# Performance work log

Hardware: AMD Instinct MI355X
Metric: run time of the kernel (lower is better)

The kernel has to match this reference:

```python
import jax, jax.numpy as jnp
import numpy as np

D_MODEL = 512
D_INNER = 1024   # expand * d_model
D_STATE = 16
D_CONV = 4
DT_RANK = 32     # ceil(d_model / 16)
N_LAYERS = 4
N_PRED_LAYERS = 2
FEAT = 128
LN_EPS = 1e-5


def _ln(x, w, b):
    m = x.mean(-1, keepdims=True)
    v = ((x - m) ** 2).mean(-1, keepdims=True)
    return (x - m) * jax.lax.rsqrt(v + LN_EPS) * w + b


def _silu(x):
    return x * jax.nn.sigmoid(x)


def _causal_conv(x, w, b):
    # depthwise causal conv1d: x (B,L,C), w (C,K), b (C,)
    K = w.shape[1]
    L = x.shape[1]
    xp = jnp.pad(x, ((0, 0), (K - 1, 0), (0, 0)))
    y = b
    for k in range(K):
        y = y + xp[:, k:k + L, :] * w[:, k]
    return y


def _mamba(x, in_w, conv_w, conv_b, xp_w, dt_w, dt_b, Alog, Dp, out_w):
    # x: (B,L,d_model)
    xz = jnp.einsum('bld,ed->ble', x, in_w)          # (B,L,2*d_inner)
    xi, z = jnp.split(xz, 2, axis=-1)
    xc = _silu(_causal_conv(xi, conv_w, conv_b))     # (B,L,d_inner)
    dbc = jnp.einsum('blc,ec->ble', xc, xp_w)        # (B,L,dt_rank+2N)
    dt = dbc[..., :DT_RANK]
    Bm = dbc[..., DT_RANK:DT_RANK + D_STATE]         # (B,L,N)
    Cm = dbc[..., DT_RANK + D_STATE:]                # (B,L,N)
    delta = jax.nn.softplus(jnp.einsum('blr,cr->blc', dt, dt_w) + dt_b)  # (B,L,d_inner)
    A = -jnp.exp(Alog)                               # (d_inner,N), negative
    dA = jnp.exp(delta[..., None] * A)               # (B,L,d_inner,N)
    dBu = delta[..., None] * Bm[:, :, None, :] * xc[..., None]

    def step(h, inp):
        dA_t, dBu_t, C_t = inp
        h = dA_t * h + dBu_t                         # (B,d_inner,N)
        y = jnp.einsum('bcn,bn->bc', h, C_t)
        return h, y

    h0 = jnp.zeros((x.shape[0], D_INNER, D_STATE), x.dtype)
    _, ys = jax.lax.scan(step, h0, (dA.transpose(1, 0, 2, 3),
                                    dBu.transpose(1, 0, 2, 3),
                                    Cm.transpose(1, 0, 2)))
    y = ys.transpose(1, 0, 2) + Dp * xc              # skip connection D*u
    y = y * _silu(z)
    return jnp.einsum('blc,dc->bld', y, out_w)


def _forward(x, inp_w, inp_b, enc_ln_w, enc_ln_b, enc_in_w, enc_conv_w, enc_conv_b,
             enc_xp_w, enc_dt_w, enc_dt_b, enc_Alog, enc_D, enc_out_w,
             fin_ln_w, fin_ln_b, prd_ln_w, prd_ln_b, prd_in_w, prd_conv_w, prd_conv_b,
             prd_xp_w, prd_dt_w, prd_dt_b, prd_Alog, prd_D, prd_out_w,
             prd_nrm_w, prd_nrm_b, prd_proj_w, prd_proj_b):
    # MambaEncoder: input_proj + n_layers pre-norm residual Mamba blocks + final LN
    h = jnp.einsum('blf,df->bld', x, inp_w) + inp_b
    for i in range(N_LAYERS):
        h = h + _mamba(_ln(h, enc_ln_w[i], enc_ln_b[i]),
                       enc_in_w[i], enc_conv_w[i], enc_conv_b[i], enc_xp_w[i],
                       enc_dt_w[i], enc_dt_b[i], enc_Alog[i], enc_D[i], enc_out_w[i])
    ctx = _ln(h, fin_ln_w, fin_ln_b)
    # MambaPredictor: small causal mamba stack + norm + proj
    p = ctx
    for i in range(N_PRED_LAYERS):
        p = p + _mamba(_ln(p, prd_ln_w[i], prd_ln_b[i]),
                       prd_in_w[i], prd_conv_w[i], prd_conv_b[i], prd_xp_w[i],
                       prd_dt_w[i], prd_dt_b[i], prd_Alog[i], prd_D[i], prd_out_w[i])
    p = _ln(p, prd_nrm_w, prd_nrm_b)
    preds = jnp.einsum('bld,ed->ble', p, prd_proj_w) + prd_proj_b
    return preds


def _mamba_params(key, n, scale=0.02):
    ks = jax.random.split(key, 6)
    arange_A = jnp.tile(jnp.log(jnp.arange(1, D_STATE + 1, dtype=jnp.float32)), (n, D_INNER, 1))
    return dict(
        in_w=jax.random.normal(ks[0], (n, 2 * D_INNER, D_MODEL)) * scale,
        conv_w=jax.random.normal(ks[1], (n, D_INNER, D_CONV)) * scale,
        conv_b=jnp.zeros((n, D_INNER)),
        xp_w=jax.random.normal(ks[2], (n, DT_RANK + 2 * D_STATE, D_INNER)) * scale,
        dt_w=jax.random.normal(ks[3], (n, D_INNER, DT_RANK)) * scale,
        dt_b=jnp.full((n, D_INNER), jnp.log(jnp.expm1(0.01))),  # inv-softplus(0.01)
        Alog=arange_A,
        D=jnp.ones((n, D_INNER)),
        out_w=jax.random.normal(ks[4], (n, D_MODEL, D_INNER)) * scale,
    )


def setup_inputs() -> dict:
    key = jax.random.key(0)
    ks = jax.random.split(key, 8)
    enc = _mamba_params(ks[0], N_LAYERS)
    prd = _mamba_params(ks[1], N_PRED_LAYERS)
    return {
        'x': jax.random.normal(ks[2], (2, 1024, FEAT), dtype=jnp.float32),
        'inp_w': jax.random.normal(ks[3], (D_MODEL, FEAT)) * 0.02,
        'inp_b': jnp.zeros((D_MODEL,)),
        'enc_ln_w': jnp.ones((N_LAYERS, D_MODEL)), 'enc_ln_b': jnp.zeros((N_LAYERS, D_MODEL)),
        'enc_in_w': enc['in_w'], 'enc_conv_w': enc['conv_w'], 'enc_conv_b': enc['conv_b'],
        'enc_xp_w': enc['xp_w'], 'enc_dt_w': enc['dt_w'], 'enc_dt_b': enc['dt_b'],
        'enc_Alog': enc['Alog'], 'enc_D': enc['D'], 'enc_out_w': enc['out_w'],
        'fin_ln_w': jnp.ones((D_MODEL,)), 'fin_ln_b': jnp.zeros((D_MODEL,)),
        'prd_ln_w': jnp.ones((N_PRED_LAYERS, D_MODEL)), 'prd_ln_b': jnp.zeros((N_PRED_LAYERS, D_MODEL)),
        'prd_in_w': prd['in_w'], 'prd_conv_w': prd['conv_w'], 'prd_conv_b': prd['conv_b'],
        'prd_xp_w': prd['xp_w'], 'prd_dt_w': prd['dt_w'], 'prd_dt_b': prd['dt_b'],
        'prd_Alog': prd['Alog'], 'prd_D': prd['D'], 'prd_out_w': prd['out_w'],
        'prd_nrm_w': jnp.ones((D_MODEL,)), 'prd_nrm_b': jnp.zeros((D_MODEL,)),
        'prd_proj_w': jax.random.normal(ks[4], (D_MODEL, D_MODEL)) * 0.02,
        'prd_proj_b': jnp.zeros((D_MODEL,)),
    }


def reference(x, inp_w, inp_b, enc_ln_w, enc_ln_b, enc_in_w, enc_conv_w, enc_conv_b,
              enc_xp_w, enc_dt_w, enc_dt_b, enc_Alog, enc_D, enc_out_w,
              fin_ln_w, fin_ln_b, prd_ln_w, prd_ln_b, prd_in_w, prd_conv_w, prd_conv_b,
              prd_xp_w, prd_dt_w, prd_dt_b, prd_Alog, prd_D, prd_out_w,
              prd_nrm_w, prd_nrm_b, prd_proj_w, prd_proj_b):
    return _forward(x, inp_w, inp_b, enc_ln_w, enc_ln_b, enc_in_w, enc_conv_w, enc_conv_b,
                    enc_xp_w, enc_dt_w, enc_dt_b, enc_Alog, enc_D, enc_out_w,
                    fin_ln_w, fin_ln_b, prd_ln_w, prd_ln_b, prd_in_w, prd_conv_w, prd_conv_b,
                    prd_xp_w, prd_dt_w, prd_dt_b, prd_Alog, prd_D, prd_out_w,
                    prd_nrm_w, prd_nrm_b, prd_proj_w, prd_proj_b)
```

## Files before the change

### kernel.cpp

```cpp
#include <hip/hip_runtime.h>
#include <hip/hip_bf16.h>

using bf16 = __hip_bfloat16;
typedef __attribute__((ext_vector_type(8))) short short8;
typedef __attribute__((ext_vector_type(4))) float f32x4;
typedef __attribute__((ext_vector_type(4))) unsigned int uint4v;

static constexpr int LB = 2;
static constexpr int LL = 1024;
static constexpr int DM = 512;
static constexpr int DI = 1024;
static constexpr int DSN = 16;
static constexpr int RK = 32;
static constexpr int MR_ROWS = LB * LL;

struct ConvArgs {
    const float* src[9];
    bf16*        dst[9];
    int          n4[9];
};

__global__ __launch_bounds__(256) void convert_bf16_multi(ConvArgs a) {
    const int s = blockIdx.y;
    const float4* __restrict__ src = (const float4*)a.src[s];
    bf16* __restrict__ dst = a.dst[s];
    const int n4 = a.n4[s];
    for (int i = blockIdx.x * 256 + threadIdx.x; i < n4; i += gridDim.x * 256) {
        float4 v = src[i];
        bf16 t[4] = {__float2bfloat16(v.x), __float2bfloat16(v.y),
                     __float2bfloat16(v.z), __float2bfloat16(v.w)};
        *(uint2*)(dst + (size_t)i * 4) = *(uint2*)t;
    }
}

__device__ __forceinline__ void ln_store(float* outrow, int tid, float a, float b) {
    ((float2*)outrow)[tid] = make_float2(a, b);
}
__device__ __forceinline__ void ln_store(bf16* outrow, int tid, float a, float b) {
    __hip_bfloat162 h;
    h.x = __float2bfloat16(a);
    h.y = __float2bfloat16(b);
    ((__hip_bfloat162*)outrow)[tid] = h;
}

template <typename T>
__global__ __launch_bounds__(256) void ln_kernel(const float* __restrict__ x,
                                                 const float* __restrict__ w,
                                                 const float* __restrict__ b,
                                                 T* __restrict__ out) {
    const int row = blockIdx.x;
    const int tid = threadIdx.x;
    const int wid = tid >> 6, lane = tid & 63;
    __shared__ float red[8];

    const float2 v = ((const float2*)(x + (size_t)row * DM))[tid];
    float s = v.x + v.y;
#pragma unroll
    for (int m = 1; m < 64; m <<= 1) s += __shfl_xor(s, m);
    if (lane == 0) red[wid] = s;
    __syncthreads();
    const float mean = (red[0] + red[1] + red[2] + red[3]) * (1.f / DM);
    const float d0 = v.x - mean, d1 = v.y - mean;
    float s2 = d0 * d0 + d1 * d1;
#pragma unroll
    for (int m = 1; m < 64; m <<= 1) s2 += __shfl_xor(s2, m);
    if (lane == 0) red[4 + wid] = s2;
    __syncthreads();
    const float var = (red[4] + red[5] + red[6] + red[7]) * (1.f / DM);
    const float rs = rsqrtf(var + 1e-5f);
    const float2 wv = ((const float2*)w)[tid];
    const float2 bv = ((const float2*)b)[tid];
    ln_store(out + (size_t)row * DM, tid, d0 * rs * wv.x + bv.x, d1 * rs * wv.y + bv.y);
}

template <int BM, int BN, int BK, int EPI>
__global__ __launch_bounds__(256) void gemm_bt(const bf16* __restrict__ A, int lda,
                                               const bf16* __restrict__ B, int ldb,
                                               float* __restrict__ C, int ldc,
                                               int K, const float* __restrict__ bias) {
    static_assert(BK == 64, "swizzle assumes 128B LDS row stride");
    constexpr int MR = (BM / 2) / 16;
    constexpr int NR = (BN / 2) / 16;
    __shared__ __align__(16) bf16 sA[BM * BK];
    __shared__ __align__(16) bf16 sB[BN * BK];

    const int tid = threadIdx.x;
    const int lane = tid & 63, wid = tid >> 6;
    const int wr = wid >> 1, wc = wid & 1;
    const int m0 = blockIdx.y * BM, n0 = blockIdx.x * BN;

    f32x4 acc[MR][NR] = {};

    constexpr int A_LD = BM * BK * 2 / (256 * 16);
    constexpr int B_LD = BN * BK * 2 / (256 * 16);
    static_assert(A_LD >= 1 && B_LD >= 1, "tile too small");

    for (int k0 = 0; k0 < K; k0 += BK) {
#pragma unroll
        for (int i = 0; i < A_LD; ++i) {
            const int byte = (tid + i * 256) * 16;
            const int row = byte / (BK * 2), colb = byte % (BK * 2);
            const int sw = colb ^ ((row & 7) << 4);
            *(uint4v*)((char*)sA + row * (BK * 2) + sw) =
                *(const uint4v*)((const char*)A + ((size_t)(m0 + row) * lda + k0) * 2 + colb);
        }
#pragma unroll
        for (int i = 0; i < B_LD; ++i) {
            const int byte = (tid + i * 256) * 16;
            const int row = byte / (BK * 2), colb = byte % (BK * 2);
            const int sw = colb ^ ((row & 7) << 4);
            *(uint4v*)((char*)sB + row * (BK * 2) + sw) =
                *(const uint4v*)((const char*)B + ((size_t)(n0 + row) * ldb + k0) * 2 + colb);
        }
        __syncthreads();
#pragma unroll
        for (int kk = 0; kk < BK; kk += 32) {
            const int kb2 = (kk + (lane >> 4) * 8) * 2;
            short8 af[MR], bfr[NR];
#pragma unroll
            for (int m = 0; m < MR; ++m) {
                const int r = wr * (BM / 2) + m * 16 + (lane & 15);
                af[m] = *(const short8*)((const char*)sA + r * (BK * 2) + (kb2 ^ ((r & 7) << 4)));
            }
#pragma unroll
            for (int n = 0; n < NR; ++n) {
                const int r = wc * (BN / 2) + n * 16 + (lane & 15);
                bfr[n] = *(const short8*)((const char*)sB + r * (BK * 2) + (kb2 ^ ((r & 7) << 4)));
            }
#pragma unroll
            for (int m = 0; m < MR; ++m) {
#pragma unroll
                for (int n = 0; n < NR; ++n) {
                    acc[m][n] = __builtin_amdgcn_mfma_f32_16x16x32_bf16(af[m], bfr[n], acc[m][n], 0, 0, 0);
                }
            }
        }
        __syncthreads();
    }

#pragma unroll
    for (int m = 0; m < MR; ++m) {
#pragma unroll
        for (int n = 0; n < NR; ++n) {
            const int col = n0 + wc * (BN / 2) + n * 16 + (lane & 15);
            const float bv = (EPI == 1) ? bias[col] : 0.f;
#pragma unroll
            for (int j = 0; j < 4; ++j) {
                const int row = m0 + wr * (BM / 2) + m * 16 + (lane >> 4) * 4 + j;
                float v = acc[m][n][j] + bv;
                float* p = C + (size_t)row * ldc + col;
                if (EPI == 3) v += *p;
                *p = v;
            }
        }
    }
}

__global__ __launch_bounds__(256) void conv_silu_T(const float* __restrict__ xz,
                                                   const float* __restrict__ cw,
                                                   const float* __restrict__ cb,
                                                   bf16* __restrict__ xc_bf,
                                                   float* __restrict__ xc_t,
                                                   float* __restrict__ zs_t) {
    const int c0 = blockIdx.x * 64;
    const int r0 = blockIdx.y * 64;
    const int bstart = (r0 >> 10) << 10;
    const int tid = threadIdx.x;

    __shared__ float sx[67 * 64];
    __shared__ float T[64 * 65];

    for (int idx = tid; idx < 67 * 16; idx += 256) {
        const int rr = idx >> 4, f4 = idx & 15;
        const int row = r0 - 3 + rr;
        float4 v = make_float4(0.f, 0.f, 0.f, 0.f);
        if (row >= bstart)
            v = *(const float4*)(xz + (size_t)row * (2 * DI) + c0 + f4 * 4);
        *(float4*)(sx + rr * 64 + f4 * 4) = v;
    }
    __syncthreads();

    const int c = tid & 63;
    const int rgrp = tid >> 6;
    const float4 w = *(const float4*)(cw + (size_t)(c0 + c) * 4);
    const float cbv = cb[c0 + c];
#pragma unroll
    for (int i = 0; i < 16; ++i) {
        const int r = rgrp + i * 4;
        float acc = cbv + w.w * sx[(r + 3) * 64 + c] + w.z * sx[(r + 2) * 64 + c]
                        + w.y * sx[(r + 1) * 64 + c] + w.x * sx[(r + 0) * 64 + c];
        const float s = acc / (1.f + expf(-acc));
        xc_bf[(size_t)(r0 + r) * DI + c0 + c] = __float2bfloat16(s);
        T[c * 65 + r] = s;
    }
    __syncthreads();
#pragma unroll
    for (int i = 0; i < 16; ++i) {
        const int idx = tid + i * 256;
        const int cc = idx >> 6, r = idx & 63;
        xc_t[(size_t)(c0 + cc) * MR_ROWS + r0 + r] = T[cc * 65 + r];
    }
    __syncthreads();

#pragma unroll
    for (int i = 0; i < 16; ++i) {
        const int r = rgrp + i * 4;
        const float zv = xz[(size_t)(r0 + r) * (2 * DI) + DI + c0 + c];
        T[c * 65 + r] = zv / (1.f + expf(-zv));
    }
    __syncthreads();
#pragma unroll
    for (int i = 0; i < 16; ++i) {
        const int idx = tid + i * 256;
        const int cc = idx >> 6, r = idx & 63;
        zs_t[(size_t)(c0 + cc) * MR_ROWS + r0 + r] = T[cc * 65 + r];
    }
}

__global__ __launch_bounds__(256) void dtproj_T(const float* __restrict__ dbc,
                                                const float* __restrict__ dtw,
                                                const float* __restrict__ dtb,
                                                float* __restrict__ delta_t) {
    const int c0 = blockIdx.x * 64;
    const int r0 = blockIdx.y * 64;
    const int tid = threadIdx.x;

    __shared__ float sdt[64 * 33];
    __shared__ float T[64 * 65];

    for (int idx = tid; idx < 64 * 32; idx += 256) {
        const int r = idx >> 5, k = idx & 31;
        sdt[r * 33 + k] = dbc[(size_t)(r0 + r) * 64 + k];
    }
    __syncthreads();

    const int c = tid & 63;
    const int rgrp = tid >> 6;
    float wv[RK];
#pragma unroll
    for (int k = 0; k < RK / 4; ++k) {
        const float4 t4 = *(const float4*)(dtw + (size_t)(c0 + c) * RK + k * 4);
        wv[4 * k] = t4.x; wv[4 * k + 1] = t4.y; wv[4 * k + 2] = t4.z; wv[4 * k + 3] = t4.w;
    }
    const float bv = dtb[c0 + c];
#pragma unroll
    for (int i = 0; i < 16; ++i) {
        const int r = rgrp + i * 4;
        float acc = bv;
#pragma unroll
        for (int k = 0; k < RK; ++k) acc = fmaf(sdt[r * 33 + k], wv[k], acc);
        T[c * 65 + r] = (acc > 20.f) ? acc : log1pf(expf(acc));
    }
    __syncthreads();
#pragma unroll
    for (int i = 0; i < 16; ++i) {
        const int idx = tid + i * 256;
        const int cc = idx >> 6, r = idx & 63;
        delta_t[(size_t)(c0 + cc) * MR_ROWS + r0 + r] = T[cc * 65 + r];
    }
}

__global__ __launch_bounds__(256) void scan_kernel(const float* __restrict__ delta_t,
                                                   const float* __restrict__ xc_t,
                                                   const float* __restrict__ zs_t,
                                                   const float* __restrict__ dbc,
                                                   const float* __restrict__ Alog,
                                                   const float* __restrict__ Dp,
                                                   bf16* __restrict__ yg) {
    const int b = blockIdx.y;
    const int c = blockIdx.x;
    const int tid = threadIdx.x;
    const int n = tid & 15;
    const int chunk = tid >> 4;
    const size_t rbase = (size_t)b * LL;
    const int t0 = chunk * 64;

    __shared__ float sdel[16 * 68], sxc[16 * 68], szs[16 * 68];
    __shared__ float sP[16][16], sS[16][16], sH[16][16];

    {
        const size_t base = (size_t)c * MR_ROWS + rbase;
        const int ch = tid >> 4, tl = (tid & 15) * 4;
        *(float4*)(sdel + ch * 68 + tl) = *(const float4*)(delta_t + base + tid * 4);
        *(float4*)(sxc  + ch * 68 + tl) = *(const float4*)(xc_t  + base + tid * 4);
        *(float4*)(szs  + ch * 68 + tl) = *(const float4*)(zs_t  + base + tid * 4);
    }

    const float a2 = -expf(Alog[(size_t)c * DSN + n]) * 1.44269504f;
    const float dp = Dp[c];
    __syncthreads();

    float h = 0.f, P = 1.f;
#pragma unroll 4
    for (int t = 0; t < 64; ++t) {
        const float d  = sdel[chunk * 68 + t];
        const float xv = sxc[chunk * 68 + t];
        const float bm = dbc[(rbase + t0 + t) * 64 + 32 + n];
        const float dA = exp2f(d * a2);
        h = fmaf(dA, h, d * bm * xv);
        P *= dA;
    }
    sP[chunk][n] = P;
    sS[chunk][n] = h;
    __syncthreads();

    if (tid < 16) {
        float hh = 0.f;
#pragma unroll
        for (int j = 0; j < 16; ++j) {
            sH[j][tid] = hh;
            hh = fmaf(sP[j][tid], hh, sS[j][tid]);
        }
    }
    __syncthreads();

    h = sH[chunk][n];
#pragma unroll 4
    for (int t = 0; t < 64; ++t) {
        const float d  = sdel[chunk * 68 + t];
        const float xv = sxc[chunk * 68 + t];
        const size_t row = rbase + t0 + t;
        const float bm = dbc[row * 64 + 32 + n];
        const float cm = dbc[row * 64 + 48 + n];
        const float dA = exp2f(d * a2);
        h = fmaf(dA, h, d * bm * xv);
        float part = h * cm;
        part += __shfl_xor(part, 1);
        part += __shfl_xor(part, 2);
        part += __shfl_xor(part, 4);
        part += __shfl_xor(part, 8);
        if (n == 0) {
            yg[row * DI + c] = __float2bfloat16((part + dp * xv) * szs[chunk * 68 + t]);
        }
    }
}

static void run_mamba_layer(hipStream_t stream, float* resid,
                            const float* ln_w, const float* ln_b,
                            const bf16* inw_bf,
                            const float* conv_w, const float* conv_b,
                            const bf16* xpw_bf,
                            const float* dt_w, const float* dt_b,
                            const float* Alog, const float* Dp,
                            const bf16* outw_bf,
                            bf16* ln_bf, float* xz, bf16* xc_bf,
                            float* xc_t, float* zs_t,
                            float* dbc, float* delta_t, bf16* yg_bf) {
    ln_kernel<bf16><<<MR_ROWS, 256, 0, stream>>>(resid, ln_w, ln_b, ln_bf);
    gemm_bt<128, 128, 64, 0><<<dim3(2 * DI / 128, MR_ROWS / 128), 256, 0, stream>>>(
        ln_bf, DM, inw_bf, DM, xz, 2 * DI, DM, nullptr);
    conv_silu_T<<<dim3(DI / 64, MR_ROWS / 64), 256, 0, stream>>>(
        xz, conv_w, conv_b, xc_bf, xc_t, zs_t);
    gemm_bt<32, 64, 64, 0><<<dim3(1, MR_ROWS / 32), 256, 0, stream>>>(
        xc_bf, DI, xpw_bf, DI, dbc, 64, DI, nullptr);
    dtproj_T<<<dim3(DI / 64, MR_ROWS / 64), 256, 0, stream>>>(dbc, dt_w, dt_b, delta_t);
    scan_kernel<<<dim3(DI, LB), 256, 0, stream>>>(delta_t, xc_t, zs_t, dbc, Alog, Dp, yg_bf);
    gemm_bt<64, 64, 64, 3><<<dim3(DM / 64, MR_ROWS / 64), 256, 0, stream>>>(
        yg_bf, DI, outw_bf, DI, resid, DM, DI, nullptr);
}

extern "C" void kernel_launch(void* const* d_in, const int* in_sizes, int n_in,
                              void* d_out, int out_size, void* d_ws, size_t ws_size,
                              hipStream_t stream) {
    const float* x         = (const float*)d_in[0];
    const float* inp_w     = (const float*)d_in[1];
    const float* inp_b     = (const float*)d_in[2];
    const float* enc_ln_w  = (const float*)d_in[3];
    const float* enc_ln_b  = (const float*)d_in[4];
    const float* enc_in_w  = (const float*)d_in[5];
    const float* enc_conv_w= (const float*)d_in[6];
    const float* enc_conv_b= (const float*)d_in[7];
    const float* enc_xp_w  = (const float*)d_in[8];
    const float* enc_dt_w  = (const float*)d_in[9];
    const float* enc_dt_b  = (const float*)d_in[10];
    const float* enc_Alog  = (const float*)d_in[11];
    const float* enc_D     = (const float*)d_in[12];
    const float* enc_out_w = (const float*)d_in[13];
    const float* fin_ln_w  = (const float*)d_in[14];
    const float* fin_ln_b  = (const float*)d_in[15];
    const float* prd_ln_w  = (const float*)d_in[16];
    const float* prd_ln_b  = (const float*)d_in[17];
    const float* prd_in_w  = (const float*)d_in[18];
    const float* prd_conv_w= (const float*)d_in[19];
    const float* prd_conv_b= (const float*)d_in[20];
    const float* prd_xp_w  = (const float*)d_in[21];
    const float* prd_dt_w  = (const float*)d_in[22];
    const float* prd_dt_b  = (const float*)d_in[23];
    const float* prd_Alog  = (const float*)d_in[24];
    const float* prd_D     = (const float*)d_in[25];
    const float* prd_out_w = (const float*)d_in[26];
    const float* prd_nrm_w = (const float*)d_in[27];
    const float* prd_nrm_b = (const float*)d_in[28];
    const float* prd_proj_w= (const float*)d_in[29];
    const float* prd_proj_b= (const float*)d_in[30];

    char* wp = (char*)d_ws;
    auto carve = [&](size_t elems, size_t esz) {
        void* p = (void*)wp;
        wp += (elems * esz + 255) & ~(size_t)255;
        return p;
    };
    bf16* x_bf     = (bf16*)carve((size_t)MR_ROWS * 128, 2);
    bf16* inpw_bf  = (bf16*)carve((size_t)DM * 128, 2);
    bf16* einw_bf  = (bf16*)carve(4ull * 2 * DI * DM, 2);
    bf16* expw_bf  = (bf16*)carve(4ull * 64 * DI, 2);
    bf16* eoutw_bf = (bf16*)carve(4ull * DM * DI, 2);
    bf16* pinw_bf  = (bf16*)carve(2ull * 2 * DI * DM, 2);
    bf16* pxpw_bf  = (bf16*)carve(2ull * 64 * DI, 2);
    bf16* poutw_bf = (bf16*)carve(2ull * DM * DI, 2);
    bf16* projw_bf = (bf16*)carve((size_t)DM * DM, 2);
    float* hbuf    = (float*)carve((size_t)MR_ROWS * DM, 4);
    float* pbuf    = (float*)carve((size_t)MR_ROWS * DM, 4);
    bf16* ln_bf    = (bf16*)carve((size_t)MR_ROWS * DM, 2);
    float* xz      = (float*)carve((size_t)MR_ROWS * 2 * DI, 4);
    bf16* xc_bf    = (bf16*)carve((size_t)MR_ROWS * DI, 2);
    float* xc_t    = (float*)carve((size_t)MR_ROWS * DI, 4);
    float* zs_t    = (float*)carve((size_t)MR_ROWS * DI, 4);
    float* dbc     = (float*)carve((size_t)MR_ROWS * 64, 4);
    float* delta_t = (float*)carve((size_t)MR_ROWS * DI, 4);
    bf16* yg_bf    = (bf16*)carve((size_t)MR_ROWS * DI, 2);

    ConvArgs ca;
    const float* csrc[9] = {x, inp_w, enc_in_w, enc_xp_w, enc_out_w,
                            prd_in_w, prd_xp_w, prd_out_w, prd_proj_w};
    bf16* cdst[9] = {x_bf, inpw_bf, einw_bf, expw_bf, eoutw_bf,
                     pinw_bf, pxpw_bf, poutw_bf, projw_bf};
    const int cn[9] = {MR_ROWS * 128, DM * 128, 4 * 2 * DI * DM, 4 * 64 * DI, 4 * DM * DI,
                       2 * 2 * DI * DM, 2 * 64 * DI, 2 * DM * DI, DM * DM};
    for (int i = 0; i < 9; ++i) { ca.src[i] = csrc[i]; ca.dst[i] = cdst[i]; ca.n4[i] = cn[i] / 4; }
    convert_bf16_multi<<<dim3(128, 9), 256, 0, stream>>>(ca);

    gemm_bt<64, 64, 64, 1><<<dim3(DM / 64, MR_ROWS / 64), 256, 0, stream>>>(
        x_bf, 128, inpw_bf, 128, hbuf, DM, 128, inp_b);

    for (int i = 0; i < 4; ++i) {
        run_mamba_layer(stream, hbuf,
                        enc_ln_w + (size_t)i * DM, enc_ln_b + (size_t)i * DM,
                        einw_bf + (size_t)i * 2 * DI * DM,
                        enc_conv_w + (size_t)i * DI * 4, enc_conv_b + (size_t)i * DI,
                        expw_bf + (size_t)i * 64 * DI,
                        enc_dt_w + (size_t)i * DI * RK, enc_dt_b + (size_t)i * DI,
                        enc_Alog + (size_t)i * DI * DSN, enc_D + (size_t)i * DI,
                        eoutw_bf + (size_t)i * DM * DI,
                        ln_bf, xz, xc_bf, xc_t, zs_t, dbc, delta_t, yg_bf);
    }

    ln_kernel<float><<<MR_ROWS, 256, 0, stream>>>(hbuf, fin_ln_w, fin_ln_b, pbuf);

    for (int i = 0; i < 2; ++i) {
        run_mamba_layer(stream, pbuf,
                        prd_ln_w + (size_t)i * DM, prd_ln_b + (size_t)i * DM,
                        pinw_bf + (size_t)i * 2 * DI * DM,
                        prd_conv_w + (size_t)i * DI * 4, prd_conv_b + (size_t)i * DI,
                        pxpw_bf + (size_t)i * 64 * DI,
                        prd_dt_w + (size_t)i * DI * RK, prd_dt_b + (size_t)i * DI,
                        prd_Alog + (size_t)i * DI * DSN, prd_D + (size_t)i * DI,
                        poutw_bf + (size_t)i * DM * DI,
                        ln_bf, xz, xc_bf, xc_t, zs_t, dbc, delta_t, yg_bf);
    }

    ln_kernel<bf16><<<MR_ROWS, 256, 0, stream>>>(pbuf, prd_nrm_w, prd_nrm_b, ln_bf);
    gemm_bt<64, 64, 64, 1><<<dim3(DM / 64, MR_ROWS / 64), 256, 0, stream>>>(
        ln_bf, DM, projw_bf, DM, (float*)d_out, DM, DM, prd_proj_b);

    (void)in_sizes; (void)n_in; (void)out_size; (void)ws_size;
}
```

Before: 748.9 us.

## Split-K x_proj GEMM, transpose B/C for coalesced scan loads, retile GEMMs

```diff
diff --git a/kernel.cpp b/kernel.cpp
--- a/kernel.cpp
+++ b/kernel.cpp
@@ -88,6 +88,7 @@
     const int lane = tid & 63, wid = tid >> 6;
     const int wr = wid >> 1, wc = wid & 1;
     const int m0 = blockIdx.y * BM, n0 = blockIdx.x * BN;
+    const int kbase = (EPI == 2) ? blockIdx.z * K : 0;
 
     f32x4 acc[MR][NR] = {};
 
@@ -95,7 +96,7 @@
     constexpr int B_LD = BN * BK * 2 / (256 * 16);
     static_assert(A_LD >= 1 && B_LD >= 1, "tile too small");
 
-    for (int k0 = 0; k0 < K; k0 += BK) {
+    for (int k0 = kbase; k0 < kbase + K; k0 += BK) {
 #pragma unroll
         for (int i = 0; i < A_LD; ++i) {
             const int byte = (tid + i * 256) * 16;
@@ -149,8 +150,12 @@
                 const int row = m0 + wr * (BM / 2) + m * 16 + (lane >> 4) * 4 + j;
                 float v = acc[m][n][j] + bv;
                 float* p = C + (size_t)row * ldc + col;
-                if (EPI == 3) v += *p;
-                *p = v;
+                if (EPI == 2) {
+                    atomicAdd(p, v);
+                } else {
+                    if (EPI == 3) v += *p;
+                    *p = v;
+                }
             }
         }
     }
@@ -220,7 +225,8 @@
 __global__ __launch_bounds__(256) void dtproj_T(const float* __restrict__ dbc,
                                                 const float* __restrict__ dtw,
                                                 const float* __restrict__ dtb,
-                                                float* __restrict__ delta_t) {
+                                                float* __restrict__ delta_t,
+                                                float* __restrict__ bct) {
     const int c0 = blockIdx.x * 64;
     const int r0 = blockIdx.y * 64;
     const int tid = threadIdx.x;
@@ -258,12 +264,19 @@
         const int cc = idx >> 6, r = idx & 63;
         delta_t[(size_t)(c0 + cc) * MR_ROWS + r0 + r] = T[cc * 65 + r];
     }
+
+    if (c0 == 0) {
+        for (int idx = tid; idx < 32 * 64; idx += 256) {
+            const int k = idx >> 6, r = idx & 63;
+            bct[(size_t)k * MR_ROWS + r0 + r] = dbc[(size_t)(r0 + r) * 64 + 32 + k];
+        }
+    }
 }
 
 __global__ __launch_bounds__(256) void scan_kernel(const float* __restrict__ delta_t,
                                                    const float* __restrict__ xc_t,
                                                    const float* __restrict__ zs_t,
-                                                   const float* __restrict__ dbc,
+                                                   const float* __restrict__ bct,
                                                    const float* __restrict__ Alog,
                                                    const float* __restrict__ Dp,
                                                    bf16* __restrict__ yg) {
@@ -288,17 +301,24 @@
 
     const float a2 = -expf(Alog[(size_t)c * DSN + n]) * 1.44269504f;
     const float dp = Dp[c];
+    const float* Bp = bct + (size_t)n * MR_ROWS + rbase + t0;
+    const float* Cp = bct + (size_t)(16 + n) * MR_ROWS + rbase + t0;
     __syncthreads();
 
     float h = 0.f, P = 1.f;
 #pragma unroll 4
-    for (int t = 0; t < 64; ++t) {
-        const float d  = sdel[chunk * 68 + t];
-        const float xv = sxc[chunk * 68 + t];
-        const float bm = dbc[(rbase + t0 + t) * 64 + 32 + n];
-        const float dA = exp2f(d * a2);
-        h = fmaf(dA, h, d * bm * xv);
-        P *= dA;
+    for (int tq = 0; tq < 16; ++tq) {
+        const float4 b4 = *(const float4*)(Bp + tq * 4);
+#pragma unroll
+        for (int j = 0; j < 4; ++j) {
+            const int t = tq * 4 + j;
+            const float d  = sdel[chunk * 68 + t];
+            const float xv = sxc[chunk * 68 + t];
+            const float bm = (j == 0) ? b4.x : (j == 1) ? b4.y : (j == 2) ? b4.z : b4.w;
+            const float dA = exp2f(d * a2);
+            h = fmaf(dA, h, d * bm * xv);
+            P *= dA;
+        }
     }
     sP[chunk][n] = P;
     sS[chunk][n] = h;
@@ -316,21 +336,27 @@
 
     h = sH[chunk][n];
 #pragma unroll 4
-    for (int t = 0; t < 64; ++t) {
-        const float d  = sdel[chunk * 68 + t];
-        const float xv = sxc[chunk * 68 + t];
-        const size_t row = rbase + t0 + t;
-        const float bm = dbc[row * 64 + 32 + n];
-        const float cm = dbc[row * 64 + 48 + n];
-        const float dA = exp2f(d * a2);
-        h = fmaf(dA, h, d * bm * xv);
-        float part = h * cm;
-        part += __shfl_xor(part, 1);
-        part += __shfl_xor(part, 2);
-        part += __shfl_xor(part, 4);
-        part += __shfl_xor(part, 8);
-        if (n == 0) {
-            yg[row * DI + c] = __float2bfloat16((part + dp * xv) * szs[chunk * 68 + t]);
+    for (int tq = 0; tq < 16; ++tq) {
+        const float4 b4 = *(const float4*)(Bp + tq * 4);
+        const float4 c4 = *(const float4*)(Cp + tq * 4);
+#pragma unroll
+        for (int j = 0; j < 4; ++j) {
+            const int t = tq * 4 + j;
+            const float d  = sdel[chunk * 68 + t];
+            const float xv = sxc[chunk * 68 + t];
+            const float bm = (j == 0) ? b4.x : (j == 1) ? b4.y : (j == 2) ? b4.z : b4.w;
+            const float cm = (j == 0) ? c4.x : (j == 1) ? c4.y : (j == 2) ? c4.z : c4.w;
+            const float dA = exp2f(d * a2);
+            h = fmaf(dA, h, d * bm * xv);
+            float part = h * cm;
+            part += __shfl_xor(part, 1);
+            part += __shfl_xor(part, 2);
+            part += __shfl_xor(part, 4);
+            part += __shfl_xor(part, 8);
+            if (n == 0) {
+                yg[(rbase + t0 + t) * DI + c] =
+                    __float2bfloat16((part + dp * xv) * szs[chunk * 68 + t]);
+            }
         }
     }
 }
@@ -345,17 +371,18 @@
                             const bf16* outw_bf,
                             bf16* ln_bf, float* xz, bf16* xc_bf,
                             float* xc_t, float* zs_t,
-                            float* dbc, float* delta_t, bf16* yg_bf) {
+                            float* dbc, float* bct, float* delta_t, bf16* yg_bf) {
     ln_kernel<bf16><<<MR_ROWS, 256, 0, stream>>>(resid, ln_w, ln_b, ln_bf);
-    gemm_bt<128, 128, 64, 0><<<dim3(2 * DI / 128, MR_ROWS / 128), 256, 0, stream>>>(
+    gemm_bt<64, 64, 64, 0><<<dim3(2 * DI / 64, MR_ROWS / 64), 256, 0, stream>>>(
         ln_bf, DM, inw_bf, DM, xz, 2 * DI, DM, nullptr);
     conv_silu_T<<<dim3(DI / 64, MR_ROWS / 64), 256, 0, stream>>>(
         xz, conv_w, conv_b, xc_bf, xc_t, zs_t);
-    gemm_bt<32, 64, 64, 0><<<dim3(1, MR_ROWS / 32), 256, 0, stream>>>(
-        xc_bf, DI, xpw_bf, DI, dbc, 64, DI, nullptr);
-    dtproj_T<<<dim3(DI / 64, MR_ROWS / 64), 256, 0, stream>>>(dbc, dt_w, dt_b, delta_t);
-    scan_kernel<<<dim3(DI, LB), 256, 0, stream>>>(delta_t, xc_t, zs_t, dbc, Alog, Dp, yg_bf);
-    gemm_bt<64, 64, 64, 3><<<dim3(DM / 64, MR_ROWS / 64), 256, 0, stream>>>(
+    hipMemsetAsync(dbc, 0, (size_t)MR_ROWS * 64 * 4, stream);
+    gemm_bt<32, 64, 64, 2><<<dim3(1, MR_ROWS / 32, 4), 256, 0, stream>>>(
+        xc_bf, DI, xpw_bf, DI, dbc, 64, DI / 4, nullptr);
+    dtproj_T<<<dim3(DI / 64, MR_ROWS / 64), 256, 0, stream>>>(dbc, dt_w, dt_b, delta_t, bct);
+    scan_kernel<<<dim3(DI, LB), 256, 0, stream>>>(delta_t, xc_t, zs_t, bct, Alog, Dp, yg_bf);
+    gemm_bt<32, 64, 64, 3><<<dim3(DM / 64, MR_ROWS / 32), 256, 0, stream>>>(
         yg_bf, DI, outw_bf, DI, resid, DM, DI, nullptr);
 }
 
@@ -417,6 +444,7 @@
     float* xc_t    = (float*)carve((size_t)MR_ROWS * DI, 4);
     float* zs_t    = (float*)carve((size_t)MR_ROWS * DI, 4);
     float* dbc     = (float*)carve((size_t)MR_ROWS * 64, 4);
+    float* bct     = (float*)carve(32ull * MR_ROWS, 4);
     float* delta_t = (float*)carve((size_t)MR_ROWS * DI, 4);
     bf16* yg_bf    = (bf16*)carve((size_t)MR_ROWS * DI, 2);
 
@@ -430,7 +458,7 @@
     for (int i = 0; i < 9; ++i) { ca.src[i] = csrc[i]; ca.dst[i] = cdst[i]; ca.n4[i] = cn[i] / 4; }
     convert_bf16_multi<<<dim3(128, 9), 256, 0, stream>>>(ca);
 
-    gemm_bt<64, 64, 64, 1><<<dim3(DM / 64, MR_ROWS / 64), 256, 0, stream>>>(
+    gemm_bt<32, 64, 64, 1><<<dim3(DM / 64, MR_ROWS / 32), 256, 0, stream>>>(
         x_bf, 128, inpw_bf, 128, hbuf, DM, 128, inp_b);
 
     for (int i = 0; i < 4; ++i) {
@@ -442,7 +470,7 @@
                         enc_dt_w + (size_t)i * DI * RK, enc_dt_b + (size_t)i * DI,
                         enc_Alog + (size_t)i * DI * DSN, enc_D + (size_t)i * DI,
                         eoutw_bf + (size_t)i * DM * DI,
-                        ln_bf, xz, xc_bf, xc_t, zs_t, dbc, delta_t, yg_bf);
+                        ln_bf, xz, xc_bf, xc_t, zs_t, dbc, bct, delta_t, yg_bf);
     }
 
     ln_kernel<float><<<MR_ROWS, 256, 0, stream>>>(hbuf, fin_ln_w, fin_ln_b, pbuf);
@@ -456,11 +484,11 @@
                         prd_dt_w + (size_t)i * DI * RK, prd_dt_b + (size_t)i * DI,
                         prd_Alog + (size_t)i * DI * DSN, prd_D + (size_t)i * DI,
                         poutw_bf + (size_t)i * DM * DI,
-                        ln_bf, xz, xc_bf, xc_t, zs_t, dbc, delta_t, yg_bf);
+                        ln_bf, xz, xc_bf, xc_t, zs_t, dbc, bct, delta_t, yg_bf);
     }
 
     ln_kernel<bf16><<<MR_ROWS, 256, 0, stream>>>(pbuf, prd_nrm_w, prd_nrm_b, ln_bf);
-    gemm_bt<64, 64, 64, 1><<<dim3(DM / 64, MR_ROWS / 64), 256, 0, stream>>>(
+    gemm_bt<32, 64, 64, 1><<<dim3(DM / 64, MR_ROWS / 32), 256, 0, stream>>>(
         ln_bf, DM, projw_bf, DM, (float*)d_out, DM, DM, prd_proj_b);
 
     (void)in_sizes; (void)n_in; (void)out_size; (void)ws_size;
```

Result: slower. 908.7 us (+21.3%).
